# Kernel optimization log

Hardware: AMD Instinct MI355X
Metric: run time of the kernel (lower is better)

Reference implementation:

```python
import jax, jax.numpy as jnp
import numpy as np


def setup_inputs() -> dict:
    key = jax.random.key(0)
    ks = jax.random.split(key, 5)
    B, N, C, H = 8, 8192, 512, 8
    scale = 1.0 / np.sqrt(C)
    return {
        "x": jax.random.normal(ks[0], (B, N, C), dtype=jnp.float32),
        "qk_w": jax.random.normal(ks[1], (2 * C, C), dtype=jnp.float32) * scale,
        "qk_b": jax.random.normal(ks[2], (2 * C,), dtype=jnp.float32) * 0.01,
        "lepe_w": jax.random.normal(ks[3], (C, 1, 3), dtype=jnp.float32) * 0.5,
        "lepe_b": jax.random.normal(ks[4], (C,), dtype=jnp.float32) * 0.01,
        "num_heads": H,
    }


def reference(x, qk_w, qk_b, lepe_w, lepe_b, num_heads):
    B, N, C = x.shape
    hd = C // num_heads
    # qk projection -> split into q, k; ELU(.)+1 feature map
    qk = x @ qk_w.T + qk_b                      # [B,N,2C]
    q = jax.nn.elu(qk[..., :C]) + 1.0
    k = jax.nn.elu(qk[..., C:]) + 1.0
    q = q.reshape(B, N, num_heads, hd).transpose(0, 2, 1, 3)  # [B,H,N,hd]
    k = k.reshape(B, N, num_heads, hd).transpose(0, 2, 1, 3)
    v = x.reshape(B, N, num_heads, hd).transpose(0, 2, 1, 3)
    # normalizer: z = 1 / (q . mean_n(k) + eps)
    k_mean = k.mean(axis=2)                                    # [B,H,hd]
    z = 1.0 / (jnp.einsum('bhnd,bhd->bhn', q, k_mean) + 1e-6)  # [B,H,N]
    # linear attention: kv = k^T v per head, then q @ kv
    kv = jnp.einsum('bhnd,bhne->bhde', k, v)                   # [B,H,hd,hd]
    attn = jnp.einsum('bhnd,bhde->bhne', q, kv) * z[..., None] # [B,H,N,hd]
    attn = attn.transpose(0, 2, 1, 3).reshape(B, N, C)
    # lepe: depthwise conv1d over tokens on v (== x after head reshape round-trip)
    vc = x.transpose(0, 2, 1)                                  # [B,C,N]
    lepe = jax.lax.conv_general_dilated(
        vc, lepe_w, window_strides=(1,), padding=((1, 1),),
        dimension_numbers=('NCH', 'OIH', 'NCH'), feature_group_count=C,
    ) + lepe_b[None, :, None]                                  # [B,C,N]
    return attn + lepe.transpose(0, 2, 1)
```

## Files before the change

### kernel.cpp

```cpp
#include <hip/hip_runtime.h>
#include <hip/hip_bf16.h>

#define B_    8
#define N_    8192
#define C_    512
#define H_    8
#define HD_   64
#define M_    (B_ * N_)
#define TWO_C 1024

typedef short short8 __attribute__((ext_vector_type(8)));
typedef float f32x4  __attribute__((ext_vector_type(4)));

__device__ __forceinline__ float bf2f(unsigned v) {
    return __uint_as_float(v << 16);
}

__device__ __forceinline__ unsigned f2bf(float f) {
    union { __hip_bfloat16 b; unsigned short u; } cv;
    cv.b = __float2bfloat16(f);
    return (unsigned)cv.u;
}

__device__ __forceinline__ uint2 pack4(float4 f) {
    uint2 r;
    r.x = f2bf(f.x) | (f2bf(f.y) << 16);
    r.y = f2bf(f.z) | (f2bf(f.w) << 16);
    return r;
}

__global__ __launch_bounds__(256) void conv_w_bf16(
    const float* __restrict__ w, unsigned short* __restrict__ wbf)
{
    const int i = (blockIdx.x * 256 + threadIdx.x) * 8;
    float4 a = *(const float4*)(w + i);
    float4 b = *(const float4*)(w + i + 4);
    uint2 pa = pack4(a), pb = pack4(b);
    *(uint4*)(wbf + i) = make_uint4(pa.x, pa.y, pb.x, pb.y);
}

__global__ __launch_bounds__(256) void conv_x_bf16(
    const float* __restrict__ x, unsigned short* __restrict__ xbf)
{
    const size_t i = ((size_t)blockIdx.x * 256 + threadIdx.x) * 8;
    float4 a = *(const float4*)(x + i);
    float4 b = *(const float4*)(x + i + 4);
    uint2 pa = pack4(a), pb = pack4(b);
    *(uint4*)(xbf + i) = make_uint4(pa.x, pa.y, pb.x, pb.y);
}

__global__ __launch_bounds__(256, 2) void gemm_qk_mfma(
    const unsigned short* __restrict__ xbf, const unsigned short* __restrict__ wbf,
    const float* __restrict__ bias,
    __hip_bfloat16* __restrict__ qws, __hip_bfloat16* __restrict__ kws)
{
    __shared__ __align__(16) unsigned short As[128 * 64];
    __shared__ __align__(16) unsigned short Bs[128 * 64];

    const int t  = threadIdx.x;
    const int wv = t >> 6;
    const int ln = t & 63;

    const int L  = blockIdx.x;
    const int rp = (L & 7) + ((L >> 6) << 3);
    const int cp = (L >> 3) & 7;
    const int m0 = rp * 128;
    const int n0 = cp * 128;

    const int wm = wv & 1, wn = wv >> 1;
    const int fr = ln & 15;
    const int qg = ln >> 4;

    const int sr = t >> 3;
    const int ss = t & 7;
    const int ds = ss ^ (sr & 7);

    f32x4 acc[4][4];
#pragma unroll
    for (int i = 0; i < 4; i++)
#pragma unroll
        for (int j = 0; j < 4; j++) acc[i][j] = {0.f, 0.f, 0.f, 0.f};

    const unsigned short* xa = xbf + (size_t)(m0 + sr) * C_ + ss * 8;
    const unsigned short* wa = wbf + (size_t)(n0 + sr) * C_ + ss * 8;
    unsigned short* const la = &As[sr * 64 + ds * 8];
    unsigned short* const lb = &Bs[sr * 64 + ds * 8];

    for (int k0 = 0; k0 < C_; k0 += 64) {
        uint4 a0 = *(const uint4*)(xa + k0);
        uint4 a1 = *(const uint4*)(xa + k0 + (size_t)32 * C_);
        uint4 a2 = *(const uint4*)(xa + k0 + (size_t)64 * C_);
        uint4 a3 = *(const uint4*)(xa + k0 + (size_t)96 * C_);
        uint4 b0 = *(const uint4*)(wa + k0);
        uint4 b1 = *(const uint4*)(wa + k0 + (size_t)32 * C_);
        uint4 b2 = *(const uint4*)(wa + k0 + (size_t)64 * C_);
        uint4 b3 = *(const uint4*)(wa + k0 + (size_t)96 * C_);
        if (k0) __syncthreads();
        *(uint4*)(la + 0 * 32 * 64) = a0;
        *(uint4*)(la + 1 * 32 * 64) = a1;
        *(uint4*)(la + 2 * 32 * 64) = a2;
        *(uint4*)(la + 3 * 32 * 64) = a3;
        *(uint4*)(lb + 0 * 32 * 64) = b0;
        *(uint4*)(lb + 1 * 32 * 64) = b1;
        *(uint4*)(lb + 2 * 32 * 64) = b2;
        *(uint4*)(lb + 3 * 32 * 64) = b3;
        __syncthreads();

        short8 af[4][2], bfr[4][2];
#pragma unroll
        for (int i = 0; i < 4; i++) {
            const int r = wm * 64 + i * 16 + fr;
#pragma unroll
            for (int kk = 0; kk < 2; kk++) {
                const int slot = (kk * 4 + qg) ^ (fr & 7);
                af[i][kk] = *(const short8*)&As[r * 64 + slot * 8];
            }
        }
#pragma unroll
        for (int j = 0; j < 4; j++) {
            const int r = wn * 64 + j * 16 + fr;
#pragma unroll
            for (int kk = 0; kk < 2; kk++) {
                const int slot = (kk * 4 + qg) ^ (fr & 7);
                bfr[j][kk] = *(const short8*)&Bs[r * 64 + slot * 8];
            }
        }
#pragma unroll
        for (int i = 0; i < 4; i++)
#pragma unroll
            for (int j = 0; j < 4; j++)
#pragma unroll
                for (int kk = 0; kk < 2; kk++)
                    acc[i][j] = __builtin_amdgcn_mfma_f32_16x16x32_bf16(
                        af[i][kk], bfr[j][kk], acc[i][j], 0, 0, 0);
    }

    __hip_bfloat16* dst;
    int oc0;
    if (n0 < C_) { dst = qws; oc0 = n0; }
    else         { dst = kws; oc0 = n0 - C_; }
    float bv[4];
#pragma unroll
    for (int j = 0; j < 4; j++) bv[j] = bias[n0 + wn * 64 + j * 16 + fr];
    const int rb = (ln >> 4) * 4;
#pragma unroll
    for (int i = 0; i < 4; i++) {
#pragma unroll
        for (int r = 0; r < 4; r++) {
            const size_t m = (size_t)(m0 + wm * 64 + i * 16 + rb + r);
#pragma unroll
            for (int j = 0; j < 4; j++) {
                const int oc = oc0 + wn * 64 + j * 16 + fr;
                float v = acc[i][j][r] + bv[j];
                v = (v > 0.f) ? (v + 1.f) : __expf(v);
                dst[m * C_ + oc] = __float2bfloat16(v);
            }
        }
    }
}

__global__ __launch_bounds__(256) void kv_partial(
    const __hip_bfloat16* __restrict__ kws, const float* __restrict__ x,
    float* __restrict__ kvT, float* __restrict__ kmean)
{
    __shared__ float kt[32][64];
    __shared__ float vt[32][64];
    const int t  = threadIdx.x;
    const int s  = blockIdx.x;
    const int bh = blockIdx.y;
    const int b  = bh >> 3, h = bh & 7;
    const int td = t >> 4, te = t & 15;
    const int kr = t >> 3;
    const int kc = (t & 7) * 8;
    const int vr = t >> 4;
    const int vc = (t & 15) * 4;

    const size_t base = (size_t)b * N_ * C_ + h * HD_;

    float acc[4][4];
    float ksum[4] = {0.f, 0.f, 0.f, 0.f};
#pragma unroll
    for (int i = 0; i < 4; i++)
#pragma unroll
        for (int j = 0; j < 4; j++) acc[i][j] = 0.f;

    const int nstart = s * (N_ / 16);
    for (int n0 = nstart; n0 < nstart + N_ / 16; n0 += 32) {
        uint4  ku = *(const uint4*)&kws[base + (size_t)(n0 + kr) * C_ + kc];
        float4 v0 = *(const float4*)&x[base + (size_t)(n0 + vr) * C_ + vc];
        float4 v1 = *(const float4*)&x[base + (size_t)(n0 + vr + 16) * C_ + vc];
        __syncthreads();
        kt[kr][kc + 0] = bf2f(ku.x & 0xffffu); kt[kr][kc + 1] = bf2f(ku.x >> 16);
        kt[kr][kc + 2] = bf2f(ku.y & 0xffffu); kt[kr][kc + 3] = bf2f(ku.y >> 16);
        kt[kr][kc + 4] = bf2f(ku.z & 0xffffu); kt[kr][kc + 5] = bf2f(ku.z >> 16);
        kt[kr][kc + 6] = bf2f(ku.w & 0xffffu); kt[kr][kc + 7] = bf2f(ku.w >> 16);
        *(float4*)&vt[vr][vc]      = v0;
        *(float4*)&vt[vr + 16][vc] = v1;
        __syncthreads();
#pragma unroll
        for (int nn = 0; nn < 32; nn++) {
            float4 kd = *(const float4*)&kt[nn][td * 4];
            float4 ve = *(const float4*)&vt[nn][te * 4];
            float kr4[4] = {kd.x, kd.y, kd.z, kd.w};
            float vr4[4] = {ve.x, ve.y, ve.z, ve.w};
#pragma unroll
            for (int i = 0; i < 4; i++)
#pragma unroll
                for (int j = 0; j < 4; j++) acc[i][j] += kr4[i] * vr4[j];
            ksum[0] += kd.x; ksum[1] += kd.y; ksum[2] += kd.z; ksum[3] += kd.w;
        }
    }

    float* kvp = kvT + (size_t)bh * HD_ * HD_;
#pragma unroll
    for (int i = 0; i < 4; i++)
#pragma unroll
        for (int j = 0; j < 4; j++)
            atomicAdd(&kvp[(te * 4 + j) * HD_ + td * 4 + i], acc[i][j]);
    if (te == 0) {
#pragma unroll
        for (int i = 0; i < 4; i++)
            atomicAdd(&kmean[bh * HD_ + td * 4 + i], ksum[i] * (1.0f / N_));
    }
}

__global__ __launch_bounds__(256, 2) void out_mfma(
    const __hip_bfloat16* __restrict__ qws, const float* __restrict__ x,
    const float* __restrict__ kvT, const float* __restrict__ kmean,
    const float* __restrict__ lw, const float* __restrict__ lb,
    float* __restrict__ out)
{
    __shared__ __align__(16) unsigned short qs[128][72];
    __shared__ __align__(16) unsigned short kvs[64][72];
    __shared__ float xs[130][68];
    __shared__ float zz[128];
    __shared__ float pz[128][2];
    __shared__ float kms[64];
    __shared__ float lw0[64], lw1[64], lw2[64], lbs[64];

    const int t  = threadIdx.x;
    const int n0 = blockIdx.x * 128;
    const int bh = blockIdx.y;
    const int b  = bh >> 3, h = bh & 7;

    {
        const __hip_bfloat16* qp = qws + ((size_t)b * N_ + n0) * C_ + h * HD_;
        for (int i = t; i < 1024; i += 256) {
            const int r = i >> 3, c8 = (i & 7) * 8;
            uint4 u = *(const uint4*)&qp[(size_t)r * C_ + c8];
            *(uint4*)&qs[r][c8] = u;
        }
    }
    {
        const float* kvp = kvT + (size_t)bh * 4096;
        for (int i = t; i < 2048; i += 256) {
            const int e = i >> 5, d0 = (i & 31) * 2;
            float2 v = *(const float2*)&kvp[e * 64 + d0];
            *(unsigned*)&kvs[e][d0] = f2bf(v.x) | (f2bf(v.y) << 16);
        }
    }
    {
        for (int i = t; i < 130 * 16; i += 256) {
            const int r = i >> 4, c4 = (i & 15) * 4;
            const int n = n0 - 1 + r;
            float4 v = make_float4(0.f, 0.f, 0.f, 0.f);
            if (n >= 0 && n < N_)
                v = *(const float4*)&x[((size_t)b * N_ + n) * C_ + h * HD_ + c4];
            *(float4*)&xs[r][c4] = v;
        }
    }
    if (t < 64) {
        const int c = h * HD_ + t;
        lw0[t] = lw[c * 3 + 0];
        lw1[t] = lw[c * 3 + 1];
        lw2[t] = lw[c * 3 + 2];
        lbs[t] = lb[c];
        kms[t] = kmean[bh * HD_ + t];
    }
    __syncthreads();

    {
        const int nn = t >> 1, d0 = (t & 1) * 32;
        float s = 0.f;
        for (int d = d0; d < d0 + 32; d++) s += bf2f(qs[nn][d]) * kms[d];
        pz[nn][t & 1] = s;
    }
    __syncthreads();
    if (t < 128) zz[t] = 1.0f / (pz[t][0] + pz[t][1] + 1e-6f);
    __syncthreads();

    const int wv = t >> 6, ln = t & 63;
    const int fr = ln & 15;
    const int fk = (ln >> 4) * 8;
    const int r0 = wv * 32;

    f32x4 acc[2][4];
#pragma unroll
    for (int bd = 0; bd < 2; bd++)
#pragma unroll
        for (int c = 0; c < 4; c++) acc[bd][c] = {0.f, 0.f, 0.f, 0.f};

    short8 af[2][2], bfr[4][2];
#pragma unroll
    for (int bd = 0; bd < 2; bd++)
#pragma unroll
        for (int kk = 0; kk < 2; kk++)
            af[bd][kk] = *(const short8*)&qs[r0 + bd * 16 + fr][kk * 32 + fk];
#pragma unroll
    for (int c = 0; c < 4; c++)
#pragma unroll
        for (int kk = 0; kk < 2; kk++)
            bfr[c][kk] = *(const short8*)&kvs[c * 16 + fr][kk * 32 + fk];
#pragma unroll
    for (int bd = 0; bd < 2; bd++)
#pragma unroll
        for (int c = 0; c < 4; c++)
#pragma unroll
            for (int kk = 0; kk < 2; kk++)
                acc[bd][c] = __builtin_amdgcn_mfma_f32_16x16x32_bf16(
                    af[bd][kk], bfr[c][kk], acc[bd][c], 0, 0, 0);

    const int rb = (ln >> 4) * 4;
#pragma unroll
    for (int bd = 0; bd < 2; bd++) {
#pragma unroll
        for (int c = 0; c < 4; c++) {
            const int e = c * 16 + fr;
            const float w0 = lw0[e], w1 = lw1[e], w2 = lw2[e], bb = lbs[e];
#pragma unroll
            for (int r = 0; r < 4; r++) {
                const int nn = r0 + bd * 16 + rb + r;
                const float le = xs[nn][e] * w0 + xs[nn + 1][e] * w1
                               + xs[nn + 2][e] * w2 + bb;
                out[((size_t)b * N_ + n0 + nn) * C_ + h * HD_ + e] =
                    acc[bd][c][r] * zz[nn] + le;
            }
        }
    }
}

extern "C" void kernel_launch(void* const* d_in, const int* in_sizes, int n_in,
                              void* d_out, int out_size, void* d_ws, size_t ws_size,
                              hipStream_t stream)
{
    const float* x      = (const float*)d_in[0];
    const float* qk_w   = (const float*)d_in[1];
    const float* qk_b   = (const float*)d_in[2];
    const float* lepe_w = (const float*)d_in[3];
    const float* lepe_b = (const float*)d_in[4];
    float* out = (float*)d_out;

    char* ws = (char*)d_ws;
    __hip_bfloat16* qws = (__hip_bfloat16*)ws;
    __hip_bfloat16* kws = qws + (size_t)M_ * C_;
    float* kvT   = (float*)(ws + 2 * (size_t)M_ * C_ * sizeof(__hip_bfloat16));
    float* kmean = kvT + (size_t)64 * HD_ * HD_;
    unsigned short* wbf = (unsigned short*)kvT;
    unsigned short* xbf = (unsigned short*)d_out;

    conv_w_bf16<<<256, 256, 0, stream>>>(qk_w, wbf);
    conv_x_bf16<<<M_ * C_ / (256 * 8), 256, 0, stream>>>(x, xbf);
    gemm_qk_mfma<<<4096, 256, 0, stream>>>(xbf, wbf, qk_b, qws, kws);
    hipMemsetAsync(kvT, 0, (size_t)(64 * HD_ * HD_ + 64 * HD_) * sizeof(float),
                   stream);
    kv_partial<<<dim3(16, 64), 256, 0, stream>>>(kws, x, kvT, kmean);
    out_mfma<<<dim3(N_ / 128, B_ * H_), 256, 0, stream>>>(
        qws, x, kvT, kmean, lepe_w, lepe_b, out);
}
```

Baseline: 514.3 us.

## Compute normalizer via MFMA, load kv fragments from global, shrink LDS for occupancy

The output kernel now loads the kv fragments straight from global memory into registers instead of staging them through shared memory. The q·k_mean normalizer is computed with an extra MFMA against a k_mean fragment held only in column 0, then shuffled, which removes two barriers and the scalar dot-product loop. The lepe input tile is stored in shared memory as bf16 rather than fp32, and launch bounds rise to 4 blocks per SM to increase occupancy. In exchange, the x values feeding the depthwise conv lose precision to bf16, and register pressure may rise under the tighter launch bound.

```diff
diff --git a/kernel.cpp b/kernel.cpp
--- a/kernel.cpp
+++ b/kernel.cpp
@@ -27,6 +27,13 @@
     r.x = f2bf(f.x) | (f2bf(f.y) << 16);
     r.y = f2bf(f.z) | (f2bf(f.w) << 16);
     return r;
+}
+
+__device__ __forceinline__ short8 pack8(float4 lo, float4 hi) {
+    uint2 a = pack4(lo), b = pack4(hi);
+    union { uint4 u; short8 s; } cv;
+    cv.u = make_uint4(a.x, a.y, b.x, b.y);
+    return cv.s;
 }
 
 __global__ __launch_bounds__(256) void conv_w_bf16(
@@ -224,24 +231,24 @@
     }
 }
 
-__global__ __launch_bounds__(256, 2) void out_mfma(
+__global__ __launch_bounds__(256, 4) void out_mfma(
     const __hip_bfloat16* __restrict__ qws, const float* __restrict__ x,
     const float* __restrict__ kvT, const float* __restrict__ kmean,
     const float* __restrict__ lw, const float* __restrict__ lb,
     float* __restrict__ out)
 {
     __shared__ __align__(16) unsigned short qs[128][72];
-    __shared__ __align__(16) unsigned short kvs[64][72];
-    __shared__ float xs[130][68];
-    __shared__ float zz[128];
-    __shared__ float pz[128][2];
-    __shared__ float kms[64];
+    __shared__ __align__(16) unsigned short xsb[130][68];
     __shared__ float lw0[64], lw1[64], lw2[64], lbs[64];
 
     const int t  = threadIdx.x;
     const int n0 = blockIdx.x * 128;
     const int bh = blockIdx.y;
     const int b  = bh >> 3, h = bh & 7;
+
+    const int wv = t >> 6, ln = t & 63;
+    const int fr = ln & 15;
+    const int fk = (ln >> 4) * 8;
 
     {
         const __hip_bfloat16* qp = qws + ((size_t)b * N_ + n0) * C_ + h * HD_;
@@ -249,14 +256,6 @@
             const int r = i >> 3, c8 = (i & 7) * 8;
             uint4 u = *(const uint4*)&qp[(size_t)r * C_ + c8];
             *(uint4*)&qs[r][c8] = u;
-        }
-    }
-    {
-        const float* kvp = kvT + (size_t)bh * 4096;
-        for (int i = t; i < 2048; i += 256) {
-            const int e = i >> 5, d0 = (i & 31) * 2;
-            float2 v = *(const float2*)&kvp[e * 64 + d0];
-            *(unsigned*)&kvs[e][d0] = f2bf(v.x) | (f2bf(v.y) << 16);
         }
     }
     {
@@ -266,7 +265,7 @@
             float4 v = make_float4(0.f, 0.f, 0.f, 0.f);
             if (n >= 0 && n < N_)
                 v = *(const float4*)&x[((size_t)b * N_ + n) * C_ + h * HD_ + c4];
-            *(float4*)&xs[r][c4] = v;
+            *(uint2*)&xsb[r][c4] = pack4(v);
         }
     }
     if (t < 64) {
@@ -275,54 +274,72 @@
         lw1[t] = lw[c * 3 + 1];
         lw2[t] = lw[c * 3 + 2];
         lbs[t] = lb[c];
-        kms[t] = kmean[bh * HD_ + t];
-    }
+    }
+
+    short8 bfr[4][2], bz[2];
+    {
+        const float* kvp = kvT + (size_t)bh * 4096;
+#pragma unroll
+        for (int c = 0; c < 4; c++)
+#pragma unroll
+            for (int kk = 0; kk < 2; kk++) {
+                const float* p = kvp + (c * 16 + fr) * 64 + kk * 32 + fk;
+                float4 lo = *(const float4*)p;
+                float4 hi = *(const float4*)(p + 4);
+                bfr[c][kk] = pack8(lo, hi);
+            }
+        const float* kmp = kmean + bh * HD_;
+        const short8 z8 = {0, 0, 0, 0, 0, 0, 0, 0};
+#pragma unroll
+        for (int kk = 0; kk < 2; kk++) {
+            const float* p = kmp + kk * 32 + fk;
+            float4 lo = *(const float4*)p;
+            float4 hi = *(const float4*)(p + 4);
+            short8 pk = pack8(lo, hi);
+            bz[kk] = (fr == 0) ? pk : z8;
+        }
+    }
+
     __syncthreads();
 
-    {
-        const int nn = t >> 1, d0 = (t & 1) * 32;
-        float s = 0.f;
-        for (int d = d0; d < d0 + 32; d++) s += bf2f(qs[nn][d]) * kms[d];
-        pz[nn][t & 1] = s;
-    }
-    __syncthreads();
-    if (t < 128) zz[t] = 1.0f / (pz[t][0] + pz[t][1] + 1e-6f);
-    __syncthreads();
-
-    const int wv = t >> 6, ln = t & 63;
-    const int fr = ln & 15;
-    const int fk = (ln >> 4) * 8;
     const int r0 = wv * 32;
 
-    f32x4 acc[2][4];
-#pragma unroll
-    for (int bd = 0; bd < 2; bd++)
+    f32x4 acc[2][4], zacc[2];
+#pragma unroll
+    for (int bd = 0; bd < 2; bd++) {
+        zacc[bd] = {0.f, 0.f, 0.f, 0.f};
 #pragma unroll
         for (int c = 0; c < 4; c++) acc[bd][c] = {0.f, 0.f, 0.f, 0.f};
-
-    short8 af[2][2], bfr[4][2];
+    }
+
+    short8 af[2][2];
 #pragma unroll
     for (int bd = 0; bd < 2; bd++)
 #pragma unroll
         for (int kk = 0; kk < 2; kk++)
             af[bd][kk] = *(const short8*)&qs[r0 + bd * 16 + fr][kk * 32 + fk];
-#pragma unroll
-    for (int c = 0; c < 4; c++)
-#pragma unroll
-        for (int kk = 0; kk < 2; kk++)
-            bfr[c][kk] = *(const short8*)&kvs[c * 16 + fr][kk * 32 + fk];
-#pragma unroll
-    for (int bd = 0; bd < 2; bd++)
+
+#pragma unroll
+    for (int bd = 0; bd < 2; bd++) {
 #pragma unroll
         for (int c = 0; c < 4; c++)
 #pragma unroll
             for (int kk = 0; kk < 2; kk++)
                 acc[bd][c] = __builtin_amdgcn_mfma_f32_16x16x32_bf16(
                     af[bd][kk], bfr[c][kk], acc[bd][c], 0, 0, 0);
+#pragma unroll
+        for (int kk = 0; kk < 2; kk++)
+            zacc[bd] = __builtin_amdgcn_mfma_f32_16x16x32_bf16(
+                af[bd][kk], bz[kk], zacc[bd], 0, 0, 0);
+    }
 
     const int rb = (ln >> 4) * 4;
 #pragma unroll
     for (int bd = 0; bd < 2; bd++) {
+        float zr[4];
+#pragma unroll
+        for (int r = 0; r < 4; r++)
+            zr[r] = 1.0f / (__shfl(zacc[bd][r], ln & 48) + 1e-6f);
 #pragma unroll
         for (int c = 0; c < 4; c++) {
             const int e = c * 16 + fr;
@@ -330,10 +347,10 @@
 #pragma unroll
             for (int r = 0; r < 4; r++) {
                 const int nn = r0 + bd * 16 + rb + r;
-                const float le = xs[nn][e] * w0 + xs[nn + 1][e] * w1
-                               + xs[nn + 2][e] * w2 + bb;
+                const float le = bf2f(xsb[nn][e]) * w0 + bf2f(xsb[nn + 1][e]) * w1
+                               + bf2f(xsb[nn + 2][e]) * w2 + bb;
                 out[((size_t)b * N_ + n0 + nn) * C_ + h * HD_ + e] =
-                    acc[bd][c][r] * zz[nn] + le;
+                    acc[bd][c][r] * zr[r] + le;
             }
         }
     }
```

Result: faster. 497.5 us (-3.3%).
